# Optimization experiments

Hardware: AMD Instinct MI355X
Metric: run time of the kernel (lower is better)

Reference implementation:

```python
import jax, jax.numpy as jnp
import numpy as np

BATCH, TIMESTEPS, DIM, OUT = 64, 512, 1024, 1024


def setup_inputs() -> dict:
    key = jax.random.key(0)
    k1, k2, k3, k4, k5, k6 = jax.random.split(key, 6)
    # glorot-normal-ish scales for params
    def glorot(k, shape):
        fan_in, fan_out = shape[0], shape[-1]
        std = (2.0 / (fan_in + fan_out)) ** 0.5
        return jax.random.normal(k, shape, dtype=jnp.float32) * std
    return {
        "inputs": jax.random.normal(k1, (BATCH, TIMESTEPS, DIM), dtype=jnp.float32),
        "prev_state": jax.random.normal(k2, (BATCH, OUT), dtype=jnp.float32),
        "Wa": glorot(k3, (OUT, OUT)),
        "Ua": glorot(k4, (DIM, OUT)),
        "Va": glorot(k5, (OUT, 1)),
        "Ba": glorot(k6, (1, OUT)),
    }


def reference(inputs, prev_state, Wa, Ua, Va, Ba):
    # WaS: [B, 1, OUT] broadcast over timesteps
    WaS = jnp.einsum("bo,op->bp", prev_state, Wa)[:, None, :]
    # UaH: [B, T, OUT]
    UaH = jnp.einsum("btd,do->bto", inputs, Ua)
    scores = jnp.tanh(UaH + WaS + Ba)            # [B, T, OUT]
    scores = jax.nn.relu(scores @ Va)            # [B, T, 1]
    sm = jax.nn.softmax(scores, axis=1)          # softmax over timesteps
    context_vector = jnp.sum(inputs * sm, axis=1)  # [B, DIM]
    return context_vector
```

## Files before the change

kernel.cpp:

```cpp
#include <hip/hip_runtime.h>


#define NBATCH 64
#define NT     512
#define NDIM   1024
#define NOUT   1024

typedef _Float16 h8 __attribute__((ext_vector_type(8)));
typedef _Float16 h4 __attribute__((ext_vector_type(4)));
typedef float f16v __attribute__((ext_vector_type(16)));

__device__ __forceinline__ float tanh_fast(float x) {
    float e = __expf(2.0f * x);
    return 1.0f - 2.0f * __builtin_amdgcn_rcpf(e + 1.0f);
}

__global__ __launch_bounds__(256) void k_pack_ua(const float* __restrict__ Ua,
                                                 _Float16* __restrict__ B16) {
    int t = blockIdx.x * 256 + threadIdx.x;
    int nn = t & 31, kg = (t >> 5) & 1, ks = (t >> 6) & 63, nt = t >> 12;
    int n = (nt << 5) + nn;
    int kbase = (ks << 4) + (kg << 3);
    h8 v;
#pragma unroll
    for (int j = 0; j < 8; ++j) v[j] = (_Float16)Ua[(size_t)(kbase + j) * 1024 + n];
    *(h8*)(B16 + ((size_t)t << 3)) = v;
}

__global__ __launch_bounds__(256) void k_was_part(const float* __restrict__ ps,
                                                  const float* __restrict__ Wa,
                                                  float* __restrict__ part) {
    int oc = blockIdx.x, b = blockIdx.y, tid = threadIdx.x;
    const float4* Wa4 = (const float4*)Wa;
    const float* psb = ps + b * 1024;
    float4 acc = {0.f, 0.f, 0.f, 0.f};
    int o0 = oc * 64;
#pragma unroll 4
    for (int o = o0; o < o0 + 64; ++o) {
        float s = psb[o];
        float4 wv = Wa4[o * 256 + tid];
        acc.x += s * wv.x; acc.y += s * wv.y; acc.z += s * wv.z; acc.w += s * wv.w;
    }
    ((float4*)part)[((oc << 6) + b) * 256 + tid] = acc;
}

__global__ __launch_bounds__(256) void k_was_reduce(const float* __restrict__ part,
                                                    const float* __restrict__ Ba,
                                                    float* __restrict__ wsWaS) {
    int b = blockIdx.x, tid = threadIdx.x;
    const float4* p4 = (const float4*)part;
    float4 acc = ((const float4*)Ba)[tid];
#pragma unroll
    for (int oc = 0; oc < 16; ++oc) {
        float4 v = p4[((oc << 6) + b) * 256 + tid];
        acc.x += v.x; acc.y += v.y; acc.z += v.z; acc.w += v.w;
    }
    ((float4*)wsWaS)[b * 256 + tid] = acc;
}

__global__ __launch_bounds__(512, 2) void k_fused_gemm(
    const float* __restrict__ inputs, const _Float16* __restrict__ B16,
    const float* __restrict__ wsWaS, const float* __restrict__ Va,
    float* __restrict__ scores)
{
    __shared__ _Float16 Ash[64 * 512];
    __shared__ float scoreSh[64];
    const int tid = threadIdx.x;
    const int lane = tid & 63, wv = tid >> 6;
    const int l31 = lane & 31, lhi = lane >> 5;
    const int r0 = blockIdx.x * 64;
    const int b = r0 >> 9;
    const int srow = tid >> 3, sq = tid & 7;

    if (tid < 64) scoreSh[tid] = 0.0f;

    const int ntb = wv << 2;
    const _Float16* bBase = B16 + ((size_t)ntb << 15) + lane * 8;

    f16v acc[2][4];
#pragma unroll
    for (int rt = 0; rt < 2; ++rt)
#pragma unroll
        for (int ct = 0; ct < 4; ++ct)
#pragma unroll
            for (int e = 0; e < 16; ++e) acc[rt][ct][e] = 0.0f;

    h8 bp[4][4];
#pragma unroll
    for (int s = 0; s < 4; ++s)
#pragma unroll
        for (int ct = 0; ct < 4; ++ct)
            bp[s][ct] = *(const h8*)(bBase + ((size_t)ct << 15) + ((size_t)s << 9));

    const int aswz = (l31 & 7) << 4;
    int aoff[4];
#pragma unroll
    for (int s = 0; s < 4; ++s) aoff[s] = (32 * s + 16 * lhi) ^ aswz;
    const char* a0b = (const char*)Ash + l31 * 1024;
    const char* a1b = a0b + 32 * 1024;
    const int swz = (srow & 7) << 4;

#pragma unroll
    for (int h = 0; h < 2; ++h) {
        if (h == 1) __syncthreads();
        {
            const float4* src = (const float4*)inputs +
                                (size_t)(r0 + srow) * 256 + (h << 7) + sq;
            char* rowb = (char*)Ash + srow * 1024;
#pragma unroll 8
            for (int jj = 0; jj < 16; ++jj) {
                float4 v = src[jj * 8];
                *(h4*)(rowb + ((64 * jj + 8 * sq) ^ swz)) =
                    (h4){ (_Float16)v.x, (_Float16)v.y, (_Float16)v.z, (_Float16)v.w };
            }
        }
        __syncthreads();

        for (int ks4 = 0; ks4 < 8; ++ks4) {
#pragma unroll
            for (int s = 0; s < 4; ++s) {
                const int ks = (h << 5) + ks4 * 4 + s;
                h8 a0 = *(const h8*)(a0b + ks4 * 128 + aoff[s]);
                h8 a1 = *(const h8*)(a1b + ks4 * 128 + aoff[s]);
#pragma unroll
                for (int ct = 0; ct < 4; ++ct) {
                    acc[0][ct] = __builtin_amdgcn_mfma_f32_32x32x16_f16(a0, bp[s][ct], acc[0][ct], 0, 0, 0);
                    acc[1][ct] = __builtin_amdgcn_mfma_f32_32x32x16_f16(a1, bp[s][ct], acc[1][ct], 0, 0, 0);
                }
                if (h == 0 || ks4 < 7) {
#pragma unroll
                    for (int ct = 0; ct < 4; ++ct)
                        bp[s][ct] = *(const h8*)(bBase + ((size_t)ct << 15) +
                                                 ((size_t)(ks + 4) << 9));
                }
            }
        }
    }

    float wsv[4], vav[4];
#pragma unroll
    for (int ct = 0; ct < 4; ++ct) {
        int n = (wv << 7) + ct * 32 + l31;
        wsv[ct] = wsWaS[b * 1024 + n];
        vav[ct] = Va[n];
    }
#pragma unroll
    for (int rt = 0; rt < 2; ++rt) {
#pragma unroll
        for (int i = 0; i < 16; ++i) {
            float s = 0.0f;
#pragma unroll
            for (int ct = 0; ct < 4; ++ct)
                s += tanh_fast(acc[rt][ct][i] + wsv[ct]) * vav[ct];
            s += __shfl_xor(s, 1);
            s += __shfl_xor(s, 2);
            s += __shfl_xor(s, 4);
            s += __shfl_xor(s, 8);
            s += __shfl_xor(s, 16);
            if (l31 == 0) {
                int row = rt * 32 + (i & 3) + ((i >> 2) << 3) + (lhi << 2);
                atomicAdd(&scoreSh[row], s);
            }
        }
    }
    __syncthreads();
    if (tid < 64) scores[r0 + tid] = fmaxf(scoreSh[tid], 0.0f);
}

__global__ __launch_bounds__(256) void k_softmax(const float* __restrict__ scores,
                                                 float* __restrict__ sm) {
    int b = blockIdx.x, tid = threadIdx.x;
    __shared__ float red[256];
    const float* sb = scores + b * 512;
    float s0 = sb[tid], s1 = sb[tid + 256];
    red[tid] = fmaxf(s0, s1);
    __syncthreads();
    for (int st = 128; st > 0; st >>= 1) {
        if (tid < st) red[tid] = fmaxf(red[tid], red[tid + st]);
        __syncthreads();
    }
    float m = red[0];
    __syncthreads();
    float e0 = __expf(s0 - m), e1 = __expf(s1 - m);
    red[tid] = e0 + e1;
    __syncthreads();
    for (int st = 128; st > 0; st >>= 1) {
        if (tid < st) red[tid] += red[tid + st];
        __syncthreads();
    }
    float inv = 1.0f / red[0];
    sm[b * 512 + tid] = e0 * inv;
    sm[b * 512 + 256 + tid] = e1 * inv;
}

__global__ __launch_bounds__(256) void k_ctx_part(const float* __restrict__ inputs,
                                                  const float* __restrict__ sm,
                                                  float* __restrict__ part) {
    int ts = blockIdx.x, b = blockIdx.y, tid = threadIdx.x;
    const float4* inF4 = (const float4*)inputs;
    float4 acc = {0.f, 0.f, 0.f, 0.f};
    int t0 = ts * 32;
#pragma unroll 8
    for (int t = t0; t < t0 + 32; ++t) {
        float wgt = sm[b * 512 + t];
        float4 x = inF4[(size_t)(b * 512 + t) * 256 + tid];
        acc.x += wgt * x.x; acc.y += wgt * x.y; acc.z += wgt * x.z; acc.w += wgt * x.w;
    }
    ((float4*)part)[((ts << 6) + b) * 256 + tid] = acc;
}

__global__ __launch_bounds__(256) void k_ctx_reduce(const float* __restrict__ part,
                                                    float* __restrict__ out) {
    int g = blockIdx.x * 256 + threadIdx.x;
    const float4* p4 = (const float4*)part;
    float4 acc = p4[g];
#pragma unroll
    for (int s = 1; s < 16; ++s) {
        float4 v = p4[s * 16384 + g];
        acc.x += v.x; acc.y += v.y; acc.z += v.z; acc.w += v.w;
    }
    ((float4*)out)[g] = acc;
}

extern "C" void kernel_launch(void* const* d_in, const int* in_sizes, int n_in,
                              void* d_out, int out_size, void* d_ws, size_t ws_size,
                              hipStream_t stream) {
    const float* inputs = (const float*)d_in[0];
    const float* prev   = (const float*)d_in[1];
    const float* Wa     = (const float*)d_in[2];
    const float* Ua     = (const float*)d_in[3];
    const float* Va     = (const float*)d_in[4];
    const float* Ba     = (const float*)d_in[5];
    float* out = (float*)d_out;

    char* ws = (char*)d_ws;
    _Float16* B16   = (_Float16*)(ws);
    float* wasPart  = (float*)(ws + (2u << 20));
    float* wsWaS    = (float*)(ws + (6u << 20));
    float* scores   = (float*)(ws + (6u << 20) + (256u << 10));
    float* sm       = (float*)(ws + (6u << 20) + (384u << 10));
    float* ctxPart  = (float*)(ws);

    hipLaunchKernelGGL(k_pack_ua,    dim3(512),    dim3(256), 0, stream, Ua, B16);
    hipLaunchKernelGGL(k_was_part,   dim3(16, 64), dim3(256), 0, stream, prev, Wa, wasPart);
    hipLaunchKernelGGL(k_was_reduce, dim3(64),     dim3(256), 0, stream, wasPart, Ba, wsWaS);
    hipLaunchKernelGGL(k_fused_gemm, dim3(512),    dim3(512), 0, stream, inputs, B16, wsWaS, Va, scores);
    hipLaunchKernelGGL(k_softmax,    dim3(64),     dim3(256), 0, stream, scores, sm);
    hipLaunchKernelGGL(k_ctx_part,   dim3(16, 64), dim3(256), 0, stream, inputs, sm, ctxPart);
    hipLaunchKernelGGL(k_ctx_reduce, dim3(64),     dim3(256), 0, stream, ctxPart, out);
}
```

Measured before the change: 330.3 us.

## Stage Ua tiles through LDS with async global_load_lds double buffering

Instead of each wave streaming its own B fragments from global memory into registers, the fused GEMM now copies B tiles into a double-buffered LDS region using global_load_lds, with a barrier per k-chunk. The output columns are processed in two passes of 512, which halves the accumulator registers per wave. The A half-tiles are restaged mid-loop and the second pass reorders K so the A half already resident in LDS is reused first. The aim is to cut VGPR pressure and overlap B fetches with MFMA work, at the price of more LDS (about 64KB for A plus 64KB for B), a __syncthreads per chunk, and possibly lower occupancy.

```diff
diff --git a/kernel.cpp b/kernel.cpp
--- a/kernel.cpp
+++ b/kernel.cpp
@@ -64,6 +64,7 @@
     float* __restrict__ scores)
 {
     __shared__ _Float16 Ash[64 * 512];
+    __shared__ _Float16 Bsh[2][32 * 512];
     __shared__ float scoreSh[64];
     const int tid = threadIdx.x;
     const int lane = tid & 63, wv = tid >> 6;
@@ -71,95 +72,104 @@
     const int r0 = blockIdx.x * 64;
     const int b = r0 >> 9;
     const int srow = tid >> 3, sq = tid & 7;
+    const int swz = (srow & 7) << 4;
 
     if (tid < 64) scoreSh[tid] = 0.0f;
 
-    const int ntb = wv << 2;
-    const _Float16* bBase = B16 + ((size_t)ntb << 15) + lane * 8;
-
-    f16v acc[2][4];
-#pragma unroll
-    for (int rt = 0; rt < 2; ++rt)
-#pragma unroll
-        for (int ct = 0; ct < 4; ++ct)
-#pragma unroll
-            for (int e = 0; e < 16; ++e) acc[rt][ct][e] = 0.0f;
-
-    h8 bp[4][4];
-#pragma unroll
-    for (int s = 0; s < 4; ++s)
-#pragma unroll
-        for (int ct = 0; ct < 4; ++ct)
-            bp[s][ct] = *(const h8*)(bBase + ((size_t)ct << 15) + ((size_t)s << 9));
+    auto stageA = [&](int h) {
+        const float4* src = (const float4*)inputs +
+                            (size_t)(r0 + srow) * 256 + (h << 7) + sq;
+        char* rowb = (char*)Ash + srow * 1024;
+#pragma unroll 8
+        for (int jj = 0; jj < 16; ++jj) {
+            float4 v = src[jj * 8];
+            *(h4*)(rowb + ((64 * jj + 8 * sq) ^ swz)) =
+                (h4){ (_Float16)v.x, (_Float16)v.y, (_Float16)v.z, (_Float16)v.w };
+        }
+    };
+    auto stageB = [&](int p, int c, int buf) {
+#pragma unroll
+        for (int i = 0; i < 2; ++i) {
+#pragma unroll
+            for (int ksl = 0; ksl < 2; ++ksl) {
+                const int ntl = 2 * wv + i;
+                const size_t goff =
+                    (((size_t)(((p << 4) + ntl) * 64 + 2 * c + ksl)) << 9) + lane * 8;
+                _Float16* dst = &Bsh[buf][(ntl * 2 + ksl) << 9];
+                __builtin_amdgcn_global_load_lds(
+                    (const __attribute__((address_space(1))) void*)(B16 + goff),
+                    (__attribute__((address_space(3))) void*)dst, 16, 0, 0);
+            }
+        }
+    };
 
     const int aswz = (l31 & 7) << 4;
-    int aoff[4];
-#pragma unroll
-    for (int s = 0; s < 4; ++s) aoff[s] = (32 * s + 16 * lhi) ^ aswz;
     const char* a0b = (const char*)Ash + l31 * 1024;
-    const char* a1b = a0b + 32 * 1024;
-    const int swz = (srow & 7) << 4;
-
-#pragma unroll
-    for (int h = 0; h < 2; ++h) {
-        if (h == 1) __syncthreads();
-        {
-            const float4* src = (const float4*)inputs +
-                                (size_t)(r0 + srow) * 256 + (h << 7) + sq;
-            char* rowb = (char*)Ash + srow * 1024;
-#pragma unroll 8
-            for (int jj = 0; jj < 16; ++jj) {
-                float4 v = src[jj * 8];
-                *(h4*)(rowb + ((64 * jj + 8 * sq) ^ swz)) =
-                    (h4){ (_Float16)v.x, (_Float16)v.y, (_Float16)v.z, (_Float16)v.w };
-            }
-        }
+
+    for (int p = 0; p < 2; ++p) {
+        f16v acc[2][2];
+#pragma unroll
+        for (int rt = 0; rt < 2; ++rt)
+#pragma unroll
+            for (int ct = 0; ct < 2; ++ct)
+#pragma unroll
+                for (int e = 0; e < 16; ++e) acc[rt][ct][e] = 0.0f;
+
+        if (p == 0) stageA(0);
+        stageB(p, p == 0 ? 0 : 16, 0);
         __syncthreads();
 
-        for (int ks4 = 0; ks4 < 8; ++ks4) {
-#pragma unroll
-            for (int s = 0; s < 4; ++s) {
-                const int ks = (h << 5) + ks4 * 4 + s;
-                h8 a0 = *(const h8*)(a0b + ks4 * 128 + aoff[s]);
-                h8 a1 = *(const h8*)(a1b + ks4 * 128 + aoff[s]);
-#pragma unroll
-                for (int ct = 0; ct < 4; ++ct) {
-                    acc[0][ct] = __builtin_amdgcn_mfma_f32_32x32x16_f16(a0, bp[s][ct], acc[0][ct], 0, 0, 0);
-                    acc[1][ct] = __builtin_amdgcn_mfma_f32_32x32x16_f16(a1, bp[s][ct], acc[1][ct], 0, 0, 0);
+        int buf = 0;
+        for (int cc = 0; cc < 32; ++cc) {
+            const int c = (p == 0) ? cc : ((cc + 16) & 31);
+            if (cc == 16) {
+                stageA(p == 0 ? 1 : 0);
+                __syncthreads();
+            }
+            if (cc < 31) stageB(p, (p == 0) ? (cc + 1) : ((cc + 17) & 31), buf ^ 1);
+#pragma unroll
+            for (int ksl = 0; ksl < 2; ++ksl) {
+                const int ks_h = (2 * c + ksl) & 31;
+                const int arow = ((ks_h >> 2) << 7) +
+                                 (((32 * (ks_h & 3)) + (lhi << 4)) ^ aswz);
+                h8 a0 = *(const h8*)(a0b + arow);
+                h8 a1 = *(const h8*)(a0b + 32768 + arow);
+                h8 bf0 = *(const h8*)&Bsh[buf][(((wv << 2) + ksl) << 9) + lane * 8];
+                h8 bf1 = *(const h8*)&Bsh[buf][(((wv << 2) + 2 + ksl) << 9) + lane * 8];
+                acc[0][0] = __builtin_amdgcn_mfma_f32_32x32x16_f16(a0, bf0, acc[0][0], 0, 0, 0);
+                acc[1][0] = __builtin_amdgcn_mfma_f32_32x32x16_f16(a1, bf0, acc[1][0], 0, 0, 0);
+                acc[0][1] = __builtin_amdgcn_mfma_f32_32x32x16_f16(a0, bf1, acc[0][1], 0, 0, 0);
+                acc[1][1] = __builtin_amdgcn_mfma_f32_32x32x16_f16(a1, bf1, acc[1][1], 0, 0, 0);
+            }
+            __syncthreads();
+            buf ^= 1;
+        }
+
+        const int c0w = p * 512 + wv * 64;
+        float wsv[2], vav[2];
+#pragma unroll
+        for (int ct = 0; ct < 2; ++ct) {
+            int n = c0w + ct * 32 + l31;
+            wsv[ct] = wsWaS[b * 1024 + n];
+            vav[ct] = Va[n];
+        }
+#pragma unroll
+        for (int rt = 0; rt < 2; ++rt) {
+#pragma unroll
+            for (int i = 0; i < 16; ++i) {
+                float s = 0.0f;
+#pragma unroll
+                for (int ct = 0; ct < 2; ++ct)
+                    s += tanh_fast(acc[rt][ct][i] + wsv[ct]) * vav[ct];
+                s += __shfl_xor(s, 1);
+                s += __shfl_xor(s, 2);
+                s += __shfl_xor(s, 4);
+                s += __shfl_xor(s, 8);
+                s += __shfl_xor(s, 16);
+                if (l31 == 0) {
+                    int row = rt * 32 + (i & 3) + ((i >> 2) << 3) + (lhi << 2);
+                    atomicAdd(&scoreSh[row], s);
                 }
-                if (h == 0 || ks4 < 7) {
-#pragma unroll
-                    for (int ct = 0; ct < 4; ++ct)
-                        bp[s][ct] = *(const h8*)(bBase + ((size_t)ct << 15) +
-                                                 ((size_t)(ks + 4) << 9));
-                }
-            }
-        }
-    }
-
-    float wsv[4], vav[4];
-#pragma unroll
-    for (int ct = 0; ct < 4; ++ct) {
-        int n = (wv << 7) + ct * 32 + l31;
-        wsv[ct] = wsWaS[b * 1024 + n];
-        vav[ct] = Va[n];
-    }
-#pragma unroll
-    for (int rt = 0; rt < 2; ++rt) {
-#pragma unroll
-        for (int i = 0; i < 16; ++i) {
-            float s = 0.0f;
-#pragma unroll
-            for (int ct = 0; ct < 4; ++ct)
-                s += tanh_fast(acc[rt][ct][i] + wsv[ct]) * vav[ct];
-            s += __shfl_xor(s, 1);
-            s += __shfl_xor(s, 2);
-            s += __shfl_xor(s, 4);
-            s += __shfl_xor(s, 8);
-            s += __shfl_xor(s, 16);
-            if (l31 == 0) {
-                int row = rt * 32 + (i & 3) + ((i >> 2) << 3) + (lhi << 2);
-                atomicAdd(&scoreSh[row], s);
             }
         }
     }
```

Measured after the change: 378.5 us. 14.6% more time.
